# Performance work log

Measured on AMD Instinct MI355X. Metric: run time of the kernel, lower is better.

## Reference

```python
import jax, jax.numpy as jnp
import numpy as np

B = 64          # batch of graphs
N_GOALS = 16
N_SHELVES = 112
N = N_GOALS + N_SHELVES   # 128 nodes per graph
L = 5           # num_layers
D = 32          # node_embedding_dim
DE = 32         # edge_embedding_dim
DT = 32         # timestep_embedding_dim
D_MSG_IN = 2 * D + DT + 1  # 97


def setup_inputs() -> dict:
    key = jax.random.key(0)
    ks = iter(jax.random.split(key, 40))
    def nrm(shape, s=0.05):
        return jax.random.normal(next(ks), shape, jnp.float32) * s
    inp = {}
    inp["pos"] = jax.random.uniform(next(ks), (B, N_SHELVES, 2), jnp.float32, -1.0, 1.0)
    inp["timesteps"] = jax.random.randint(next(ks), (B,), 0, 1000)
    inp["goal_pos"] = jax.random.uniform(next(ks), (N_GOALS, 2), jnp.float32, -1.0, 1.0)
    inp["W_hin"] = nrm((2, D));            inp["b_hin"] = nrm((D,))
    inp["W_msg1"] = nrm((L, D_MSG_IN, DE)); inp["b_msg1"] = nrm((L, DE))
    inp["W_msg2"] = nrm((L, DE, DE));       inp["b_msg2"] = nrm((L, DE))
    inp["W_att"] = nrm((L, DE, 1));         inp["b_att"] = nrm((L, 1))
    inp["W_pos1"] = nrm((L, DE, DE));       inp["b_pos1"] = nrm((L, DE))
    inp["W_pos2"] = nrm((L, DE, 1));        inp["b_pos2"] = nrm((L, 1))
    inp["W_node1"] = nrm((L - 1, DE + D, D)); inp["b_node1"] = nrm((L - 1, D))
    inp["W_node2"] = nrm((L - 1, D, D));      inp["b_node2"] = nrm((L - 1, D))
    inp["W_t"] = nrm((L - 1, DT, DT));        inp["b_t"] = nrm((L - 1, DT))
    return inp


def _forward(pos, timesteps, goal_pos, W_hin, b_hin, W_msg1, b_msg1, W_msg2, b_msg2,
             W_att, b_att, W_pos1, b_pos1, W_pos2, b_pos2,
             W_node1, b_node1, W_node2, b_node2, W_t, b_t):
    silu = jax.nn.silu
    b = pos.shape[0]
    n_g = goal_pos.shape[0]
    n_sh = pos.shape[1]
    n = n_g + n_sh
    num_layers = W_msg1.shape[0]

    # fully-connected edge template per graph (PyG: edge_index[0]=src=row, edge_index[1]=dst=col)
    src_l = jnp.repeat(jnp.arange(n), n)
    dst_l = jnp.tile(jnp.arange(n), n)
    offs = (jnp.arange(b) * n)[:, None]
    src = (offs + src_l[None, :]).reshape(-1)   # [b*n*n]
    dst = (offs + dst_l[None, :]).reshape(-1)
    e_batch = jnp.repeat(jnp.arange(b), n * n)  # batch[edge_index[0]]

    # node one-hot features: goals [1,0], shelves [0,1]
    h0 = jnp.concatenate([
        jnp.tile(jnp.array([1.0, 0.0], jnp.float32), (n_g, 1)),
        jnp.tile(jnp.array([0.0, 1.0], jnp.float32), (n_sh, 1)),
    ], axis=0)                                   # [n, 2]
    x = jnp.tile(h0, (b, 1))                     # [b*n, 2]

    # node positions: goal positions (shared template) then shelf positions
    p = jnp.concatenate([jnp.broadcast_to(goal_pos, (b, n_g, 2)), pos], axis=1).reshape(-1, 2)

    # sinusoidal timestep embedding
    dt = b_t.shape[-1]
    half = dt // 2
    freqs = jnp.exp(-jnp.log(10000.0) * jnp.arange(half, dtype=jnp.float32) / half)
    ang = timesteps.astype(jnp.float32)[:, None] * freqs[None, :]
    temb = jnp.concatenate([jnp.cos(ang), jnp.sin(ang)], axis=-1)  # [b, dt]

    h = x @ W_hin + b_hin  # [b*n, D]

    for i in range(num_layers):
        te = temb[e_batch]                       # [E, dt]
        pd = p[dst] - p[src]                     # pos_i - pos_j
        radial = jnp.sum(pd * pd, axis=-1, keepdims=True)
        pd = pd / (jax.lax.stop_gradient(jnp.sqrt(radial)) + 1e-6)
        m = jnp.concatenate([h[dst], h[src], radial, te], axis=-1)  # [E, 97]
        m = silu(m @ W_msg1[i] + b_msg1[i])
        m = silu(m @ W_msg2[i] + b_msg2[i])
        m = m * jax.nn.sigmoid(m @ W_att[i] + b_att[i])             # attention gate
        pw = silu(m @ W_pos1[i] + b_pos1[i]) @ W_pos2[i] + b_pos2[i]  # [E, 1]
        aggr_h = jax.ops.segment_sum(m, dst, num_segments=b * n)    # scatter-add
        # scatter-mean: every node receives exactly n incoming edges (fully connected incl. self-loop)
        aggr_p = jax.ops.segment_sum(pd * pw, dst, num_segments=b * n) / n
        if i < num_layers - 1:
            u = silu(jnp.concatenate([h, aggr_h], axis=-1) @ W_node1[i] + b_node1[i])
            u = u @ W_node2[i] + b_node2[i]
            h = jnp.where(u > 0, u, 0.01 * u) + h   # LeakyReLU + residual
            temb = silu(temb @ W_t[i] + b_t[i])
        p = aggr_p + p

    return p.reshape(b, n, 2)[:, n_g:, :].reshape(pos.shape)


def reference(pos, timesteps, goal_pos, W_hin, b_hin, W_msg1, b_msg1, W_msg2, b_msg2,
              W_att, b_att, W_pos1, b_pos1, W_pos2, b_pos2,
              W_node1, b_node1, W_node2, b_node2, W_t, b_t):
    return _forward(pos, timesteps, goal_pos, W_hin, b_hin, W_msg1, b_msg1, W_msg2, b_msg2,
                    W_att, b_att, W_pos1, b_pos1, W_pos2, b_pos2,
                    W_node1, b_node1, W_node2, b_node2, W_t, b_t)
```

## Files before the change

### kernel.cpp

```cpp
#include <hip/hip_runtime.h>
#include <hip/hip_bf16.h>

constexpr int B = 64;
constexpr int NG = 16;
constexpr int NSH = 112;
constexpr int N = 128;
constexpr int NN = B * N;
constexpr int L = 5;

constexpr int OFF_H     = 0;
constexpr int OFF_P     = OFF_H + NN * 32;
constexpr int OFF_TEMB0 = OFF_P + NN * 2;
constexpr int OFF_TEMB1 = OFF_TEMB0 + B * 32;
constexpr int OFF_HA    = OFF_TEMB1 + B * 32;
constexpr int OFF_HB    = OFF_HA + NN * 32;
constexpr int OFF_AGH   = OFF_HB + NN * 32;
constexpr int OFF_AGP   = OFF_AGH + NN * 32;

typedef __attribute__((ext_vector_type(8))) short bf16x8;
typedef __attribute__((ext_vector_type(4))) float f32x4;

__device__ __forceinline__ float fsigmoid(float x) {
    return __builtin_amdgcn_rcpf(1.0f + __expf(-x));
}
__device__ __forceinline__ float fsilu(float x) { return x * fsigmoid(x); }
__device__ __forceinline__ short f2bfs(float f) {
    union { __hip_bfloat16 b; short s; } u; u.b = __float2bfloat16(f); return u.s;
}
__device__ __forceinline__ float bf2f(unsigned short u) {
    union { unsigned int i; float f; } v; v.i = ((unsigned int)u) << 16; return v.f;
}
__device__ __forceinline__ unsigned int pk_trunc(float lo, float hi) {
    union { float f; unsigned int u; } a, b;
    a.f = hi; b.f = lo;
    return __builtin_amdgcn_perm(a.u, b.u, 0x07060302u);
}

__global__ __launch_bounds__(256) void setup_kernel(
    const float* __restrict__ pos, const int* __restrict__ timesteps,
    const float* __restrict__ goal_pos,
    const float* __restrict__ W_hin, const float* __restrict__ b_hin,
    float* __restrict__ ws)
{
    int idx = blockIdx.x * 256 + threadIdx.x;

    if (idx < NN * 32) {
        int c = idx & 31; int node = idx >> 5; int local = node & 127;
        int row = (local < NG) ? 0 : 1;
        ws[OFF_H + idx] = W_hin[row * 32 + c] + b_hin[c];
        return;
    }
    idx -= NN * 32;
    if (idx < NN * 2) {
        int d = idx & 1; int node = idx >> 1; int g = node >> 7; int local = node & 127;
        float v = (local < NG) ? goal_pos[local * 2 + d]
                               : pos[(g * NSH + (local - NG)) * 2 + d];
        ws[OFF_P + idx] = v;
        return;
    }
    idx -= NN * 2;
    if (idx < B * 32) {
        int j = idx & 31; int g = idx >> 5;
        float t = (float)timesteps[g];
        int jj = (j < 16) ? j : (j - 16);
        float freq = expf(-logf(10000.0f) * (float)jj / 16.0f);
        float ang = t * freq;
        ws[OFF_TEMB0 + idx] = (j < 16) ? cosf(ang) : sinf(ang);
    }
}

__global__ __launch_bounds__(256) void pre_kernel(
    float* __restrict__ R,
    const float* __restrict__ W_msg1, const float* __restrict__ b_msg1,
    const float* __restrict__ tembIn, int layer)
{
    int tid = blockIdx.x * 256 + threadIdx.x;
    int c = tid & 31; int node = tid >> 5; int g = node >> 7;
    const float* __restrict__ W1 = W_msg1 + layer * 97 * 32;
    float accA = b_msg1[layer * 32 + c];
    float accB = 0.f;
#pragma unroll
    for (int k = 0; k < 32; ++k) {
        float hk = R[OFF_H + node * 32 + k];
        accA += hk * W1[k * 32 + c];
        accB += hk * W1[(32 + k) * 32 + c];
    }
#pragma unroll
    for (int k = 0; k < 32; ++k)
        accA += tembIn[g * 32 + k] * W1[(65 + k) * 32 + c];
    R[OFF_HA + tid] = accA;
    ((unsigned short*)(R + OFF_HB))[tid] = (unsigned short)f2bfs(accB);
}

__global__ __attribute__((amdgpu_flat_work_group_size(256, 256)))
__attribute__((amdgpu_waves_per_eu(2, 4))) void edge_kernel(
    float* __restrict__ R,
    const float* __restrict__ W_msg1,
    const float* __restrict__ W_msg2, const float* __restrict__ b_msg2,
    const float* __restrict__ W_att, const float* __restrict__ b_att,
    const float* __restrict__ W_pos1, const float* __restrict__ b_pos1,
    const float* __restrict__ W_pos2, const float* __restrict__ b_pos2,
    float* __restrict__ aggh, float* __restrict__ aggp, int layer)
{
    __shared__ unsigned short sHBh[128 * 40];
    __shared__ float sPx[128], sPy[128];
    __shared__ unsigned int mbuf[4 * 16 * 20];
    __shared__ float2 spn[4][64];

    const int t = threadIdx.x;
    const int bx = blockIdx.x;
    const int g = bx >> 5;
    const int gbase = g * 128;

    const unsigned short* HBH = (const unsigned short*)(R + OFF_HB);
#pragma unroll
    for (int ch = 0; ch < 2; ++ch) {
        int chunk = t + ch * 256;
        int row = chunk >> 2, g4 = chunk & 3;
        uint4 v = *(const uint4*)(HBH + (gbase + row) * 32 + (g4 << 3));
        *(uint4*)(sHBh + row * 40 + (g4 << 3)) = v;
    }
    if (t < 128) {
        sPx[t] = R[OFF_P + (gbase + t) * 2];
        sPy[t] = R[OFF_P + (gbase + t) * 2 + 1];
    }
    __syncthreads();

    const int lane = t & 63, w = t >> 6;
    const int c = lane & 15;
    const int rg = lane >> 4;
    const int kk = rg << 3;
    const int dloc = ((bx & 31) << 2) | w;
    const int dstNode = gbase + dloc;

    const float* __restrict__ Wm2L = W_msg2 + layer * 1024;
    const float* __restrict__ Wp1L = W_pos1 + layer * 1024;
    bf16x8 WB1c0, WB1c1, WBpc0, WBpc1, WBac;
#pragma unroll
    for (int j = 0; j < 8; ++j) {
        WB1c0[j] = f2bfs(Wm2L[(kk + j) * 32 + c]);
        WB1c1[j] = f2bfs(Wm2L[(kk + j) * 32 + c + 16]);
        int pk = ((kk + j) & 1) * 16 + ((kk + j) >> 1);
        WBpc0[j] = f2bfs(Wp1L[pk * 32 + c]);
        WBpc1[j] = f2bfs(Wp1L[pk * 32 + c + 16]);
        WBac[j]  = f2bfs(W_att[layer * 32 + pk]);
    }

    float vha[8], vwr[8];
    {
        const float* haR = R + OFF_HA + dstNode * 32 + kk;
        const float* wrR = W_msg1 + layer * 97 * 32 + 64 * 32 + kk;
#pragma unroll
        for (int j = 0; j < 8; ++j) { vha[j] = haR[j]; vwr[j] = wrR[j]; }
    }
    const float batt   = b_att[layer];
    const float vbm20  = b_msg2[layer * 32 + c], vbm21 = b_msg2[layer * 32 + c + 16];
    const float vbp10  = b_pos1[layer * 32 + c], vbp11 = b_pos1[layer * 32 + c + 16];
    const float vwp20  = W_pos2[layer * 32 + c], vwp21 = W_pos2[layer * 32 + c + 16];
    const float bp2    = b_pos2[layer];
    const float pxd = R[OFF_P + dstNode * 2], pyd = R[OFF_P + dstNode * 2 + 1];

    unsigned int* mb = mbuf + w * 16 * 20;

    float aghc0 = 0.f, aghc1 = 0.f, apx = 0.f, apy = 0.f, spnx = 0.f, spny = 0.f;

#pragma unroll 1
    for (int half = 0; half < 2; ++half) {
        const int src = (half << 6) + lane;
        const float dx = pxd - sPx[src];
        const float dy = pyd - sPy[src];
        const float radial = dx * dx + dy * dy;
        const float inv = __builtin_amdgcn_rcpf(__builtin_amdgcn_sqrtf(radial) + 1e-6f);
        const float pnx = dx * inv, pny = dy * inv;
        spnx += pnx; spny += pny;
        spn[w][lane] = (float2){pnx, pny};

#pragma unroll
        for (int tt = 0; tt < 4; ++tt) {
            const float rad_t = __shfl(radial, c + (tt << 4));
            uint4 hraw = *(const uint4*)(sHBh + ((half << 6) + c + (tt << 4)) * 40 + kk);
            const unsigned short* hs = (const unsigned short*)&hraw;
            float x[8];
#pragma unroll
            for (int j = 0; j < 8; ++j)
                x[j] = fsilu(vha[j] + bf2f(hs[j]) + rad_t * vwr[j]);
            union { unsigned int u[4]; bf16x8 v; } af;
#pragma unroll
            for (int d = 0; d < 4; ++d) af.u[d] = pk_trunc(x[2 * d], x[2 * d + 1]);
            f32x4 a0 = (f32x4){vbm20, vbm20, vbm20, vbm20};
            f32x4 a1 = (f32x4){vbm21, vbm21, vbm21, vbm21};
            a0 = __builtin_amdgcn_mfma_f32_16x16x32_bf16(af.v, WB1c0, a0, 0, 0, 0);
            a1 = __builtin_amdgcn_mfma_f32_16x16x32_bf16(af.v, WB1c1, a1, 0, 0, 0);

            float s0[4], s1[4];
#pragma unroll
            for (int j = 0; j < 4; ++j) {
                s0[j] = fsilu(a0[j]);
                s1[j] = fsilu(a1[j]);
                mb[((rg << 2) + j) * 20 + c] = pk_trunc(s0[j], s1[j]);
            }

            union { uint4 u; bf16x8 v; } qa;
            qa.u = *(const uint4*)(mb + c * 20 + (rg << 2));
            f32x4 za = (f32x4){batt, batt, batt, batt};
            f32x4 z0 = (f32x4){0.f, 0.f, 0.f, 0.f};
            f32x4 z1 = (f32x4){0.f, 0.f, 0.f, 0.f};
            za = __builtin_amdgcn_mfma_f32_16x16x32_bf16(qa.v, WBac,  za, 0, 0, 0);
            z0 = __builtin_amdgcn_mfma_f32_16x16x32_bf16(qa.v, WBpc0, z0, 0, 0, 0);
            z1 = __builtin_amdgcn_mfma_f32_16x16x32_bf16(qa.v, WBpc1, z1, 0, 0, 0);
#pragma unroll
            for (int j = 0; j < 4; ++j) {
                const float att = fsigmoid(za[j]);
                aghc0 += att * s0[j];
                aghc1 += att * s1[j];
                const float q0 = fsilu(att * z0[j] + vbp10);
                const float q1 = fsilu(att * z1[j] + vbp11);
                const float pwp = q0 * vwp20 + q1 * vwp21;
                const float2 pn = spn[w][(tt << 4) + (rg << 2) + j];
                apx += pwp * pn.x;
                apy += pwp * pn.y;
            }
        }
    }

    aghc0 += __shfl_xor(aghc0, 16); aghc0 += __shfl_xor(aghc0, 32);
    aghc1 += __shfl_xor(aghc1, 16); aghc1 += __shfl_xor(aghc1, 32);
#pragma unroll
    for (int off = 1; off < 64; off <<= 1) {
        apx  += __shfl_xor(apx, off);
        apy  += __shfl_xor(apy, off);
        spnx += __shfl_xor(spnx, off);
        spny += __shfl_xor(spny, off);
    }
    if (lane < 16)       aggh[dstNode * 32 + lane] = aghc0;
    else if (lane < 32)  aggh[dstNode * 32 + lane] = aghc1;
    if (lane == 0) {
        aggp[dstNode * 2]     = (apx + bp2 * spnx) * (1.0f / 128.0f);
        aggp[dstNode * 2 + 1] = (apy + bp2 * spny) * (1.0f / 128.0f);
    }
}

__global__ __launch_bounds__(256) void node_kernel(
    float* __restrict__ ws,
    const float* __restrict__ W_node1, const float* __restrict__ b_node1,
    const float* __restrict__ W_node2, const float* __restrict__ b_node2,
    const float* __restrict__ W_t, const float* __restrict__ b_t,
    const float* __restrict__ W_msg1, const float* __restrict__ b_msg1,
    int layer)
{
    __shared__ float sIn[8][64];
    __shared__ float sU1[8][32];
    __shared__ float sHn[8][32];
    __shared__ float sTold[32], sTnew[32];

    const int tid = blockIdx.x * 256 + threadIdx.x;
    const int c = tid & 31;
    const int node = tid >> 5;
    const int ln = (threadIdx.x >> 5) & 7;
    const int g = node >> 7;

    const float* __restrict__ Wn1 = W_node1 + layer * 2048;
    const float* __restrict__ Wn2 = W_node2 + layer * 1024;

    sIn[ln][c]      = ws[OFF_H + node * 32 + c];
    sIn[ln][32 + c] = ws[OFF_AGH + node * 32 + c];
    if (threadIdx.x < 32)
        sTold[threadIdx.x] = ws[((layer & 1) ? OFF_TEMB1 : OFF_TEMB0) + g * 32 + threadIdx.x];
    __syncthreads();

    float acc = b_node1[layer * 32 + c];
#pragma unroll
    for (int k = 0; k < 32; ++k)
        acc += sIn[ln][k] * Wn1[k * 32 + c] + sIn[ln][32 + k] * Wn1[(32 + k) * 32 + c];
    sU1[ln][c] = fsilu(acc);
    if (threadIdx.x < 32) {
        const float* Wt = W_t + layer * 1024;
        float a2 = b_t[layer * 32 + threadIdx.x];
#pragma unroll
        for (int k = 0; k < 32; ++k) a2 += sTold[k] * Wt[k * 32 + threadIdx.x];
        sTnew[threadIdx.x] = fsilu(a2);
    }
    __syncthreads();

    float u = b_node2[layer * 32 + c];
#pragma unroll
    for (int k = 0; k < 32; ++k) u += sU1[ln][k] * Wn2[k * 32 + c];
    const float hn = (u > 0.f ? u : 0.01f * u) + sIn[ln][c];
    ws[OFF_H + node * 32 + c] = hn;
    sHn[ln][c] = hn;

    if (c < 2)
        ws[OFF_P + node * 2 + c] += ws[OFF_AGP + node * 2 + c];
    if ((blockIdx.x & 15) == 0 && threadIdx.x < 32)
        ws[((layer & 1) ? OFF_TEMB0 : OFF_TEMB1) + g * 32 + threadIdx.x] = sTnew[threadIdx.x];
    __syncthreads();

    const float* __restrict__ W1 = W_msg1 + (layer + 1) * 97 * 32;
    float accA = b_msg1[(layer + 1) * 32 + c];
    float accB = 0.f;
#pragma unroll
    for (int k = 0; k < 32; ++k) {
        const float hk = sHn[ln][k];
        accA += hk * W1[k * 32 + c];
        accB += hk * W1[(32 + k) * 32 + c];
    }
#pragma unroll
    for (int k = 0; k < 32; ++k)
        accA += sTnew[k] * W1[(65 + k) * 32 + c];
    ws[OFF_HA + node * 32 + c] = accA;
    ((unsigned short*)(ws + OFF_HB))[node * 32 + c] = (unsigned short)f2bfs(accB);
}

__global__ __launch_bounds__(256) void out_kernel(const float* __restrict__ R,
                                                  float* __restrict__ out)
{
    const int o = blockIdx.x * 256 + threadIdx.x;
    if (o >= B * NSH * 2) return;
    const int d = o & 1;
    const int s = (o >> 1) % NSH;
    const int b = (o >> 1) / NSH;
    const int node = b * 128 + NG + s;
    out[o] = R[OFF_P + node * 2 + d] + R[OFF_AGP + node * 2 + d];
}

extern "C" void kernel_launch(void* const* d_in, const int* in_sizes, int n_in,
                              void* d_out, int out_size, void* d_ws, size_t ws_size,
                              hipStream_t stream)
{
    const float* pos      = (const float*)d_in[0];
    const int*   tsteps   = (const int*)d_in[1];
    const float* goal_pos = (const float*)d_in[2];
    const float* W_hin    = (const float*)d_in[3];
    const float* b_hin    = (const float*)d_in[4];
    const float* W_msg1   = (const float*)d_in[5];
    const float* b_msg1   = (const float*)d_in[6];
    const float* W_msg2   = (const float*)d_in[7];
    const float* b_msg2   = (const float*)d_in[8];
    const float* W_att    = (const float*)d_in[9];
    const float* b_att    = (const float*)d_in[10];
    const float* W_pos1   = (const float*)d_in[11];
    const float* b_pos1   = (const float*)d_in[12];
    const float* W_pos2   = (const float*)d_in[13];
    const float* b_pos2   = (const float*)d_in[14];
    const float* W_node1  = (const float*)d_in[15];
    const float* b_node1  = (const float*)d_in[16];
    const float* W_node2  = (const float*)d_in[17];
    const float* b_node2  = (const float*)d_in[18];
    const float* W_t      = (const float*)d_in[19];
    const float* b_t      = (const float*)d_in[20];

    float* ws = (float*)d_ws;

    constexpr int setup_threads = NN * 32 + NN * 2 + B * 32;
    setup_kernel<<<(setup_threads + 255) / 256, 256, 0, stream>>>(
        pos, tsteps, goal_pos, W_hin, b_hin, ws);
    pre_kernel<<<NN * 32 / 256, 256, 0, stream>>>(ws, W_msg1, b_msg1, ws + OFF_TEMB0, 0);

    for (int l = 0; l < L; ++l) {
        edge_kernel<<<2048, 256, 0, stream>>>(ws, W_msg1, W_msg2, b_msg2, W_att, b_att,
                                              W_pos1, b_pos1, W_pos2, b_pos2,
                                              ws + OFF_AGH, ws + OFF_AGP, l);
        if (l < L - 1)
            node_kernel<<<NN * 32 / 256, 256, 0, stream>>>(ws, W_node1, b_node1, W_node2,
                                                           b_node2, W_t, b_t, W_msg1, b_msg1, l);
    }
    out_kernel<<<(B * NSH * 2 + 255) / 256, 256, 0, stream>>>(ws, (float*)d_out);
}
```

Measured before the change: 308.3 us.

## Rewrite node kernel with bf16 MFMA per 16-node wave and fold output into edge kernel

The node update MLPs and the next layer's message projections are rewritten as bf16 MFMA 16x16x32 ops, with one 64-thread wave handling 16 nodes. This replaces the scalar per-channel FMA loops that re-read weights from global memory. The final layer's edge kernel now writes the output positions directly, which removes the separate out_kernel launch. The cost is bf16 rounding of the hidden states and weights inside the node MLP, which may lower accuracy, and the time-embedding MLP is now recomputed redundantly in every block.

```diff
diff --git a/kernel.cpp b/kernel.cpp
--- a/kernel.cpp
+++ b/kernel.cpp
@@ -100,7 +100,8 @@
     const float* __restrict__ W_att, const float* __restrict__ b_att,
     const float* __restrict__ W_pos1, const float* __restrict__ b_pos1,
     const float* __restrict__ W_pos2, const float* __restrict__ b_pos2,
-    float* __restrict__ aggh, float* __restrict__ aggp, int layer)
+    float* __restrict__ aggh, float* __restrict__ aggp,
+    float* __restrict__ out, int layer)
 {
     __shared__ unsigned short sHBh[128 * 40];
     __shared__ float sPx[128], sPy[128];
@@ -232,15 +233,21 @@
         spnx += __shfl_xor(spnx, off);
         spny += __shfl_xor(spny, off);
     }
-    if (lane < 16)       aggh[dstNode * 32 + lane] = aghc0;
-    else if (lane < 32)  aggh[dstNode * 32 + lane] = aghc1;
-    if (lane == 0) {
-        aggp[dstNode * 2]     = (apx + bp2 * spnx) * (1.0f / 128.0f);
-        aggp[dstNode * 2 + 1] = (apy + bp2 * spny) * (1.0f / 128.0f);
-    }
-}
-
-__global__ __launch_bounds__(256) void node_kernel(
+    if (layer < L - 1) {
+        if (lane < 16)       aggh[dstNode * 32 + lane] = aghc0;
+        else if (lane < 32)  aggh[dstNode * 32 + lane] = aghc1;
+        if (lane == 0) {
+            aggp[dstNode * 2]     = (apx + bp2 * spnx) * (1.0f / 128.0f);
+            aggp[dstNode * 2 + 1] = (apy + bp2 * spny) * (1.0f / 128.0f);
+        }
+    } else if (lane == 0 && dloc >= NG) {
+        out[(g * NSH + (dloc - NG)) * 2]     = pxd + (apx + bp2 * spnx) * (1.0f / 128.0f);
+        out[(g * NSH + (dloc - NG)) * 2 + 1] = pyd + (apy + bp2 * spny) * (1.0f / 128.0f);
+    }
+}
+
+__global__ __attribute__((amdgpu_flat_work_group_size(64, 64)))
+__attribute__((amdgpu_waves_per_eu(2, 4))) void node_kernel(
     float* __restrict__ ws,
     const float* __restrict__ W_node1, const float* __restrict__ b_node1,
     const float* __restrict__ W_node2, const float* __restrict__ b_node2,
@@ -248,79 +255,124 @@
     const float* __restrict__ W_msg1, const float* __restrict__ b_msg1,
     int layer)
 {
-    __shared__ float sIn[8][64];
-    __shared__ float sU1[8][32];
-    __shared__ float sHn[8][32];
-    __shared__ float sTold[32], sTnew[32];
-
-    const int tid = blockIdx.x * 256 + threadIdx.x;
-    const int c = tid & 31;
-    const int node = tid >> 5;
-    const int ln = (threadIdx.x >> 5) & 7;
-    const int g = node >> 7;
+    __shared__ float sH[16][36];
+    __shared__ float sAG[16][36];
+    __shared__ unsigned int mb[16 * 20];
+
+    const int lane = threadIdx.x;
+    const int bx = blockIdx.x;
+    const int nbase = bx << 4;
+    const int g = bx >> 3;
+    const int c = lane & 15, rg = lane >> 4, kk = rg << 3;
+
+    {
+        const int row = lane >> 2, seg = lane & 3;
+        const float* hsrc = ws + OFF_H + (nbase + row) * 32 + (seg << 3);
+        const float* asrc = ws + OFF_AGH + (nbase + row) * 32 + (seg << 3);
+#pragma unroll
+        for (int j = 0; j < 8; ++j) {
+            sH[row][(seg << 3) + j]  = hsrc[j];
+            sAG[row][(seg << 3) + j] = asrc[j];
+        }
+    }
 
     const float* __restrict__ Wn1 = W_node1 + layer * 2048;
     const float* __restrict__ Wn2 = W_node2 + layer * 1024;
-
-    sIn[ln][c]      = ws[OFF_H + node * 32 + c];
-    sIn[ln][32 + c] = ws[OFF_AGH + node * 32 + c];
-    if (threadIdx.x < 32)
-        sTold[threadIdx.x] = ws[((layer & 1) ? OFF_TEMB1 : OFF_TEMB0) + g * 32 + threadIdx.x];
-    __syncthreads();
-
-    float acc = b_node1[layer * 32 + c];
-#pragma unroll
-    for (int k = 0; k < 32; ++k)
-        acc += sIn[ln][k] * Wn1[k * 32 + c] + sIn[ln][32 + k] * Wn1[(32 + k) * 32 + c];
-    sU1[ln][c] = fsilu(acc);
-    if (threadIdx.x < 32) {
-        const float* Wt = W_t + layer * 1024;
-        float a2 = b_t[layer * 32 + threadIdx.x];
-#pragma unroll
-        for (int k = 0; k < 32; ++k) a2 += sTold[k] * Wt[k * 32 + threadIdx.x];
-        sTnew[threadIdx.x] = fsilu(a2);
-    }
-    __syncthreads();
-
-    float u = b_node2[layer * 32 + c];
-#pragma unroll
-    for (int k = 0; k < 32; ++k) u += sU1[ln][k] * Wn2[k * 32 + c];
-    const float hn = (u > 0.f ? u : 0.01f * u) + sIn[ln][c];
-    ws[OFF_H + node * 32 + c] = hn;
-    sHn[ln][c] = hn;
-
-    if (c < 2)
-        ws[OFF_P + node * 2 + c] += ws[OFF_AGP + node * 2 + c];
-    if ((blockIdx.x & 15) == 0 && threadIdx.x < 32)
-        ws[((layer & 1) ? OFF_TEMB0 : OFF_TEMB1) + g * 32 + threadIdx.x] = sTnew[threadIdx.x];
-    __syncthreads();
-
-    const float* __restrict__ W1 = W_msg1 + (layer + 1) * 97 * 32;
-    float accA = b_msg1[(layer + 1) * 32 + c];
-    float accB = 0.f;
-#pragma unroll
-    for (int k = 0; k < 32; ++k) {
-        const float hk = sHn[ln][k];
-        accA += hk * W1[k * 32 + c];
-        accB += hk * W1[(32 + k) * 32 + c];
-    }
-#pragma unroll
-    for (int k = 0; k < 32; ++k)
-        accA += sTnew[k] * W1[(65 + k) * 32 + c];
-    ws[OFF_HA + node * 32 + c] = accA;
-    ((unsigned short*)(ws + OFF_HB))[node * 32 + c] = (unsigned short)f2bfs(accB);
-}
-
-__global__ __launch_bounds__(256) void out_kernel(const float* __restrict__ R,
-                                                  float* __restrict__ out)
-{
-    const int o = blockIdx.x * 256 + threadIdx.x;
-    if (o >= B * NSH * 2) return;
-    const int d = o & 1;
-    const int s = (o >> 1) % NSH;
-    const int b = (o >> 1) / NSH;
-    const int node = b * 128 + NG + s;
-    out[o] = R[OFF_P + node * 2 + d] + R[OFF_AGP + node * 2 + d];
+    const float* __restrict__ W1  = W_msg1 + (layer + 1) * 97 * 32;
+    bf16x8 B1[2][2], B2[2], Ba[2], Bb[2];
+#pragma unroll
+    for (int j = 0; j < 8; ++j) {
+        const int pk = ((kk + j) & 1) * 16 + ((kk + j) >> 1);
+#pragma unroll
+        for (int nh = 0; nh < 2; ++nh) {
+            B1[0][nh][j] = f2bfs(Wn1[(kk + j) * 32 + nh * 16 + c]);
+            B1[1][nh][j] = f2bfs(Wn1[(32 + kk + j) * 32 + nh * 16 + c]);
+            B2[nh][j]    = f2bfs(Wn2[pk * 32 + nh * 16 + c]);
+            Ba[nh][j]    = f2bfs(W1[pk * 32 + nh * 16 + c]);
+            Bb[nh][j]    = f2bfs(W1[(32 + pk) * 32 + nh * 16 + c]);
+        }
+    }
+
+    const int c2 = lane & 31;
+    const float* __restrict__ tin = ws + ((layer & 1) ? OFF_TEMB1 : OFF_TEMB0) + g * 32;
+    const float* __restrict__ Wt = W_t + layer * 1024;
+    float a2 = b_t[layer * 32 + c2];
+#pragma unroll
+    for (int k = 0; k < 32; ++k) a2 += tin[k] * Wt[k * 32 + c2];
+    const float tnew = fsilu(a2);
+    float tv = b_msg1[(layer + 1) * 32 + c2];
+#pragma unroll
+    for (int k = 0; k < 32; ++k) tv += __shfl(tnew, k) * W1[(65 + k) * 32 + c2];
+    if ((bx & 7) == 0 && lane < 32)
+        ws[((layer & 1) ? OFF_TEMB0 : OFF_TEMB1) + g * 32 + lane] = tnew;
+
+    union { unsigned int u[4]; bf16x8 v; } A0, A1;
+#pragma unroll
+    for (int d = 0; d < 4; ++d) {
+        A0.u[d] = pk_trunc(sH[c][kk + 2 * d],  sH[c][kk + 2 * d + 1]);
+        A1.u[d] = pk_trunc(sAG[c][kk + 2 * d], sAG[c][kk + 2 * d + 1]);
+    }
+    f32x4 u1[2];
+#pragma unroll
+    for (int nh = 0; nh < 2; ++nh) {
+        const float bb = b_node1[layer * 32 + nh * 16 + c];
+        f32x4 acc = (f32x4){bb, bb, bb, bb};
+        acc = __builtin_amdgcn_mfma_f32_16x16x32_bf16(A0.v, B1[0][nh], acc, 0, 0, 0);
+        acc = __builtin_amdgcn_mfma_f32_16x16x32_bf16(A1.v, B1[1][nh], acc, 0, 0, 0);
+        u1[nh] = acc;
+    }
+
+#pragma unroll
+    for (int j = 0; j < 4; ++j)
+        mb[((rg << 2) + j) * 20 + c] = pk_trunc(fsilu(u1[0][j]), fsilu(u1[1][j]));
+    union { uint4 q; bf16x8 v; } qa;
+    qa.q = *(const uint4*)(mb + c * 20 + (rg << 2));
+    f32x4 u2[2];
+#pragma unroll
+    for (int nh = 0; nh < 2; ++nh) {
+        const float bb = b_node2[layer * 32 + nh * 16 + c];
+        f32x4 acc = (f32x4){bb, bb, bb, bb};
+        u2[nh] = __builtin_amdgcn_mfma_f32_16x16x32_bf16(qa.v, B2[nh], acc, 0, 0, 0);
+    }
+
+    float hp0[4], hp1[4];
+#pragma unroll
+    for (int j = 0; j < 4; ++j) {
+        const int row = (rg << 2) + j;
+        const float h0 = sH[row][c], h1 = sH[row][c + 16];
+        const float v0 = u2[0][j], v1 = u2[1][j];
+        hp0[j] = (v0 > 0.f ? v0 : 0.01f * v0) + h0;
+        hp1[j] = (v1 > 0.f ? v1 : 0.01f * v1) + h1;
+        ws[OFF_H + (nbase + row) * 32 + c]      = hp0[j];
+        ws[OFF_H + (nbase + row) * 32 + c + 16] = hp1[j];
+        mb[row * 20 + c] = pk_trunc(hp0[j], hp1[j]);
+    }
+
+    qa.q = *(const uint4*)(mb + c * 20 + (rg << 2));
+    f32x4 ha[2], hb[2];
+    {
+        f32x4 zz = (f32x4){0.f, 0.f, 0.f, 0.f};
+#pragma unroll
+        for (int nh = 0; nh < 2; ++nh) {
+            ha[nh] = __builtin_amdgcn_mfma_f32_16x16x32_bf16(qa.v, Ba[nh], zz, 0, 0, 0);
+            hb[nh] = __builtin_amdgcn_mfma_f32_16x16x32_bf16(qa.v, Bb[nh], zz, 0, 0, 0);
+        }
+    }
+    const float tv0 = __shfl(tv, c), tv1 = __shfl(tv, c + 16);
+    unsigned short* HBH = (unsigned short*)(ws + OFF_HB);
+#pragma unroll
+    for (int j = 0; j < 4; ++j) {
+        const int node = nbase + (rg << 2) + j;
+        ws[OFF_HA + node * 32 + c]      = ha[0][j] + tv0;
+        ws[OFF_HA + node * 32 + c + 16] = ha[1][j] + tv1;
+        HBH[node * 32 + c]      = (unsigned short)f2bfs(hb[0][j]);
+        HBH[node * 32 + c + 16] = (unsigned short)f2bfs(hb[1][j]);
+    }
+
+    if (lane < 32) {
+        const int node = nbase + (lane >> 1), d = lane & 1;
+        ws[OFF_P + node * 2 + d] += ws[OFF_AGP + node * 2 + d];
+    }
 }
 
 extern "C" void kernel_launch(void* const* d_in, const int* in_sizes, int n_in,
@@ -359,10 +411,10 @@
     for (int l = 0; l < L; ++l) {
         edge_kernel<<<2048, 256, 0, stream>>>(ws, W_msg1, W_msg2, b_msg2, W_att, b_att,
                                               W_pos1, b_pos1, W_pos2, b_pos2,
-                                              ws + OFF_AGH, ws + OFF_AGP, l);
+                                              ws + OFF_AGH, ws + OFF_AGP,
+                                              (float*)d_out, l);
         if (l < L - 1)
-            node_kernel<<<NN * 32 / 256, 256, 0, stream>>>(ws, W_node1, b_node1, W_node2,
-                                                           b_node2, W_t, b_t, W_msg1, b_msg1, l);
-    }
-    out_kernel<<<(B * NSH * 2 + 255) / 256, 256, 0, stream>>>(ws, (float*)d_out);
-}
+            node_kernel<<<512, 64, 0, stream>>>(ws, W_node1, b_node1, W_node2,
+                                                b_node2, W_t, b_t, W_msg1, b_msg1, l);
+    }
+}
```

After: 293.4 us. 1.05x faster.
